# Kernel tuning notes

Hardware: AMD Instinct MI355X
Metric: run time of the kernel (lower is better)

The kernel has to match this reference:

```python
import jax, jax.numpy as jnp
import numpy as np

ALPHA = 0.5
BETA = 0.25
D_AGG = 0.5          # delta_aggregation
D_DIS = 3.0          # delta_discrimination
OHEM_RATIO = 3.0
MAX_INST = 8         # max instance label (labels in 1..MAX_INST, 0 = background)
SMOOTH = 1e-3


def _aggr_discr(text, kernel, embed):
    # text, kernel: [HW] int32 instance labels; embed: [4, HW] float
    inst = jnp.arange(1, MAX_INST + 1)                              # [I]
    kmask = (kernel[None, :] == inst[:, None]).astype(embed.dtype)  # [I, HW]
    tmask = (text[None, :] == inst[:, None]).astype(embed.dtype)   # [I, HW]
    kcnt = kmask.sum(1)                                             # [I]
    tcnt = tmask.sum(1)
    valid = ((kcnt > 0) & (tcnt > 0)).astype(embed.dtype)           # [I]
    # per-instance kernel-mean embedding (segment mean)
    avgs = (kmask @ embed.T) / jnp.maximum(kcnt, 1.0)[:, None]      # [I, 4]
    # aggregation: per-pixel distance to the mean of its text instance
    avgs_full = jnp.concatenate([jnp.zeros((1, 4), embed.dtype), avgs], 0)  # row 0 = bg
    pix_avg = avgs_full[text]                                       # [HW, 4]
    sq = jnp.sum((embed.T - pix_avg) ** 2, axis=1)
    dist = jnp.sqrt(sq + 1e-12) - D_AGG
    lg = jnp.log1p(jnp.maximum(dist, 0.0) ** 2)                     # [HW]
    aggr_i = (tmask @ lg) / jnp.maximum(tcnt, 1.0)                  # [I]
    n = valid.sum()
    loss_aggr = jnp.where(n > 0, (aggr_i * valid).sum() / jnp.maximum(n, 1.0), 0.0)
    # discrimination: pairwise hinge between valid kernel means
    pairv = jnp.triu(valid[:, None] * valid[None, :], k=1)          # [I, I]
    sq_ij = jnp.sum((avgs[:, None, :] - avgs[None, :, :]) ** 2, axis=-1)
    d_ij = jnp.sqrt(jnp.where(pairv > 0, sq_ij, 1.0))               # safe sqrt
    L = jnp.log1p(jnp.maximum(D_DIS - d_ij, 0.0) ** 2)
    denom = n * (n - 1)
    loss_discr = jnp.where(n > 1, (L * pairv).sum() / jnp.maximum(denom, 1.0), 0.0)
    return loss_aggr, loss_discr


def _ohem(score, gt_text, gt_mask):
    # score, gt_text, gt_mask: [HW] float
    pos = gt_text > 0.5
    maskpos = gt_mask > 0.5
    pos_num = (pos & maskpos).sum()
    neg = ~pos
    neg_num = jnp.minimum((pos_num * OHEM_RATIO).astype(jnp.int32), neg.sum())
    neg_sc = jnp.where(neg, score, -jnp.inf)
    srt = -jnp.sort(-neg_sc)                                        # descending
    thr = srt[jnp.clip(neg_num - 1, 0, score.shape[0] - 1)]
    samp = ((score >= thr) | pos) & maskpos
    fallback = (pos_num == 0) | (neg_num == 0)
    return jnp.where(fallback, maskpos, samp).astype(score.dtype)


def _dice(pred_logits, target, mask):
    # all [N, HW]
    p = jax.nn.sigmoid(pred_logits) * mask
    t = (target > 0.5).astype(p.dtype) * mask
    a = jnp.sum(p * t, 1) + SMOOTH
    b = jnp.sum(p * p, 1) + SMOOTH
    c = jnp.sum(t * t, 1) + SMOOTH
    return 1.0 - 2.0 * a / (b + c)


def reference(preds, gt_texts, gt_kernels, gt_mask):
    N, C, H, W = preds.shape
    HW = H * W
    pred_text = preds[:, 0].reshape(N, HW)
    pred_kernel = preds[:, 1].reshape(N, HW)
    embed = preds[:, 2:].reshape(N, 4, HW)
    t = gt_texts.reshape(N, HW)
    k = gt_kernels.reshape(N, HW)
    m = gt_mask.reshape(N, HW).astype(preds.dtype)
    tf = t.astype(preds.dtype)
    kf = k.astype(preds.dtype)
    loss_aggr, loss_discr = jax.vmap(_aggr_discr)(t, k, embed)
    samp = jax.vmap(_ohem)(jax.lax.stop_gradient(pred_text), tf, m)
    loss_text = _dice(pred_text, tf, samp)
    samp_k = (tf > 0.5).astype(preds.dtype) * m
    loss_kernel = _dice(pred_kernel, kf, samp_k)
    # reduction='mean' then coefs [1, alpha, beta, beta]
    return jnp.stack([
        loss_text.mean(),
        ALPHA * loss_kernel.mean(),
        BETA * loss_aggr.mean(),
        BETA * loss_discr.mean(),
    ])


def setup_inputs() -> dict:
    key = jax.random.key(0)
    k1, k2, k3, k4 = jax.random.split(key, 4)
    N, H, W = 16, 512, 512
    preds = jax.random.normal(k1, (N, 6, H, W), dtype=jnp.float32)
    gt_texts = jax.random.randint(k2, (N, H, W), 0, 9, dtype=jnp.int32)
    gt_kernels = jax.random.randint(k3, (N, H, W), 0, 9, dtype=jnp.int32)
    gt_mask = jax.random.randint(k4, (N, H, W), 0, 2, dtype=jnp.int32)
    return {"preds": preds, "gt_texts": gt_texts, "gt_kernels": gt_kernels, "gt_mask": gt_mask}
```

## Files before the change

### kernel.cpp

```cpp
#include <hip/hip_runtime.h>
#include <math.h>

#define HW (512 * 512)
#define NB 16
#define NTHR 256
#define GXS 64
#define CH 4
#define NSEG 256
#define SEGSZ 1024
#define REP 16

#define OFF_ACC    0
#define ACC_STRIDE (NB * 52)
#define OFF_PACC   (OFF_ACC + REP * ACC_STRIDE)
#define PACC_STRIDE (NB * 4)
#define OFF_HISTFB (OFF_PACC + REP * PACC_STRIDE)
#define OFF_NEGMX  (OFF_HISTFB + 4 * 16 * 256)
#define ZERO_WORDS (OFF_NEGMX + NB * REP)
#define OFF_TBL    ZERO_WORDS
#define OFF_THR    (OFF_TBL + 16 * 45)
#define OFF_FB     (OFF_THR + 16)
#define OFF_NVAL   (OFF_FB + 16)
#define OFF_DISCR  (OFF_NVAL + 16)
#define OFF_PREFIX (OFF_DISCR + 16)
#define OFF_KKC    (OFF_PREFIX + 16)
#define OFF_NEGC   (OFF_KKC + 16)
#define OFF_CNTS   (OFF_NEGC + 16)
#define OFF_KEYS   (OFF_CNTS + NB * NSEG)
#define WS_FULL_BYTES ((size_t)(OFF_KEYS + NB * HW) * 4)


__device__ __forceinline__ unsigned fmap(float f) {
    unsigned u = __float_as_uint(f);
    return (u & 0x80000000u) ? ~u : (u | 0x80000000u);
}
__device__ __forceinline__ float funmap(unsigned u) {
    return (u & 0x80000000u) ? __uint_as_float(u & 0x7FFFFFFFu)
                             : __uint_as_float(~u);
}
__device__ __forceinline__ float wred(float x) {
#pragma unroll
    for (int o = 32; o; o >>= 1) x += __shfl_xor(x, o);
    return x;
}
__device__ __forceinline__ unsigned wredu(unsigned x) {
#pragma unroll
    for (int o = 32; o; o >>= 1) x += __shfl_xor(x, o);
    return x;
}
__device__ __forceinline__ unsigned wredumax(unsigned x) {
#pragma unroll
    for (int o = 32; o; o >>= 1) x = max(x, (unsigned)__shfl_xor((int)x, o));
    return x;
}

__global__ __launch_bounds__(NTHR, 2) void k_stats(const float* __restrict__ preds,
                        const int* __restrict__ text,
                        const int* __restrict__ kern,
                        const int* __restrict__ mask,
                        unsigned* __restrict__ wsu, int do_compact) {
    float* wsf = (float*)wsu;
    const int b = blockIdx.y;
    const int tid = threadIdx.x;
    const int lane = tid & 63;
    const unsigned long long lmask = (1ull << lane) - 1ull;
    __shared__ float sacc[52];
    if (tid < 52) sacc[tid] = 0.f;
    __syncthreads();

    const int* tb = text + b * HW;
    const int* kb = kern + b * HW;
    const int* mb = mask + b * HW;
    const float* p0 = preds + (size_t)(b * 6 + 0) * HW;
    const float* p1 = preds + (size_t)(b * 6 + 1) * HW;
    const float* e0 = preds + (size_t)(b * 6 + 2) * HW;
    const float* e1 = e0 + HW;
    const float* e2 = e0 + 2 * HW;
    const float* e3 = e0 + 3 * HW;

    const int seg = blockIdx.x * 4 + (tid >> 6);
    unsigned* keys = wsu + OFF_KEYS + (size_t)b * HW + (size_t)seg * SEGSZ;
    unsigned segoff = 0;
    unsigned mkAll = 0u;

    float ks[32];
#pragma unroll
    for (int i = 0; i < 32; i++) ks[i] = 0.f;
    float r_ak = 0.f, r_bk = 0.f, r_ck = 0.f;
    unsigned kcW[8] = {0, 0, 0, 0, 0, 0, 0, 0};
    unsigned tcW[8] = {0, 0, 0, 0, 0, 0, 0, 0};
    unsigned posW = 0;

#pragma unroll 1
    for (int c = 0; c < CH; c++) {
        const int base = blockIdx.x * (NTHR * 4 * CH) + c * (NTHR * 4) + tid * 4;
        const int4 t4 = *(const int4*)(tb + base);
        const int4 k4 = *(const int4*)(kb + base);
        const int4 m4 = *(const int4*)(mb + base);
        const float4 s4 = *(const float4*)(p0 + base);
        const float4 q4 = *(const float4*)(p1 + base);
        const float4 a4 = *(const float4*)(e0 + base);
        const float4 b4 = *(const float4*)(e1 + base);
        const float4 c4 = *(const float4*)(e2 + base);
        const float4 d4 = *(const float4*)(e3 + base);

#define PIX(T, K, M, Q, A, B, C, D) do {                                     \
        bool pos_ = (T) > 0, mp_ = (M) > 0;                                  \
        float sm_ = (pos_ && mp_) ? 1.f : 0.f;                               \
        float sg_ = 1.f / (1.f + expf(-(Q)));                                \
        float ik_ = ((K) > 0) ? 1.f : 0.f;                                   \
        r_ak += sm_ * sg_ * ik_;                                             \
        r_bk += sm_ * sg_ * sg_;                                             \
        r_ck += sm_ * ik_;                                                   \
        posW += (unsigned)__popcll(__ballot(pos_ && mp_));                   \
        _Pragma("unroll")                                                    \
        for (int i_ = 0; i_ < 8; i_++) {                                     \
            bool hit_ = ((K) == i_ + 1);                                     \
            kcW[i_] += (unsigned)__popcll(__ballot(hit_));                   \
            tcW[i_] += (unsigned)__popcll(__ballot((T) == i_ + 1));          \
            float h_ = hit_ ? 1.f : 0.f;                                     \
            ks[i_ * 4 + 0] += h_ * (A);                                      \
            ks[i_ * 4 + 1] += h_ * (B);                                      \
            ks[i_ * 4 + 2] += h_ * (C);                                      \
            ks[i_ * 4 + 3] += h_ * (D);                                      \
        }                                                                    \
    } while (0)

        PIX(t4.x, k4.x, m4.x, q4.x, a4.x, b4.x, c4.x, d4.x);
        PIX(t4.y, k4.y, m4.y, q4.y, a4.y, b4.y, c4.y, d4.y);
        PIX(t4.z, k4.z, m4.z, q4.z, a4.z, b4.z, c4.z, d4.z);
        PIX(t4.w, k4.w, m4.w, q4.w, a4.w, b4.w, c4.w, d4.w);
#undef PIX

        const unsigned long long m0 = __ballot(t4.x == 0);
        const unsigned long long m1 = __ballot(t4.y == 0);
        const unsigned long long m2 = __ballot(t4.z == 0);
        const unsigned long long m3 = __ballot(t4.w == 0);
        const unsigned c0 = (unsigned)__popcll(m0), c1 = (unsigned)__popcll(m1);
        const unsigned c2 = (unsigned)__popcll(m2), c3 = (unsigned)__popcll(m3);
        if (do_compact) {
            if (t4.x == 0) keys[segoff + (unsigned)__popcll(m0 & lmask)] = fmap(s4.x);
            if (t4.y == 0) keys[segoff + c0 + (unsigned)__popcll(m1 & lmask)] = fmap(s4.y);
            if (t4.z == 0) keys[segoff + c0 + c1 + (unsigned)__popcll(m2 & lmask)] = fmap(s4.z);
            if (t4.w == 0) keys[segoff + c0 + c1 + c2 + (unsigned)__popcll(m3 & lmask)] = fmap(s4.w);
        }
        segoff += c0 + c1 + c2 + c3;
        unsigned mk = 0u;
        if (t4.x == 0) mk = max(mk, ~fmap(s4.x));
        if (t4.y == 0) mk = max(mk, ~fmap(s4.y));
        if (t4.z == 0) mk = max(mk, ~fmap(s4.z));
        if (t4.w == 0) mk = max(mk, ~fmap(s4.w));
        mkAll = max(mkAll, mk);
    }

    if (lane == 0) wsu[OFF_CNTS + b * NSEG + seg] = segoff;
    mkAll = wredumax(mkAll);
    if (lane == 0 && mkAll)
        atomicMax(&wsu[OFF_NEGMX + b * REP + (blockIdx.x & (REP - 1))], mkAll);

#pragma unroll
    for (int i = 0; i < 32; i++) {
        float v = wred(ks[i]);
        if (lane == 0) atomicAdd(&sacc[16 + i], v);
    }
    {
        float v = wred(r_ak); if (lane == 0) atomicAdd(&sacc[49], v);
        v = wred(r_bk); if (lane == 0) atomicAdd(&sacc[50], v);
        v = wred(r_ck); if (lane == 0) atomicAdd(&sacc[51], v);
    }
    if (lane == 0) {
#pragma unroll
        for (int i = 0; i < 8; i++) {
            atomicAdd(&sacc[i], (float)kcW[i]);
            atomicAdd(&sacc[8 + i], (float)tcW[i]);
        }
        atomicAdd(&sacc[48], (float)posW);
    }
    __syncthreads();
    if (tid < 52) {
        const int rep = blockIdx.x & (REP - 1);
        atomicAdd(&wsf[OFF_ACC + rep * ACC_STRIDE + b * 52 + tid], sacc[tid]);
    }
}

__global__ void k_sel(unsigned* __restrict__ wsu, int do_select) {
    float* wsf = (float*)wsu;
    const int b = blockIdx.x;
    const int tid = threadIdx.x;
    const int lane = tid & 63;
    __shared__ float s_acc[52];
    __shared__ float s_avg[8][4];
    __shared__ int s_valid[8];
    __shared__ unsigned s_hist[256];
    __shared__ unsigned s_negtot;
    __shared__ unsigned s_kk, s_prefix;

    if (tid < 52) {
        float v = 0.f;
#pragma unroll
        for (int r = 0; r < REP; r++) v += wsf[OFF_ACC + r * ACC_STRIDE + b * 52 + tid];
        s_acc[tid] = v;
    }
    if (tid == 0) s_negtot = 0u;
    __syncthreads();

    const unsigned myc = wsu[OFF_CNTS + b * NSEG + tid];
    {
        unsigned cw = wredu(myc);
        if (lane == 0) atomicAdd(&s_negtot, cw);
    }
    if (tid < 8) {
        float kcf = s_acc[tid];
        float tcf = s_acc[8 + tid];
        int valid = (kcf > 0.f && tcf > 0.f) ? 1 : 0;
        float inv = 1.f / fmaxf(kcf, 1.f);
        float w = valid ? 1.f / fmaxf(tcf, 1.f) : 0.f;
#pragma unroll
        for (int c = 0; c < 4; c++) {
            float a = s_acc[16 + tid * 4 + c] * inv;
            s_avg[tid][c] = a;
            wsf[OFF_TBL + b * 45 + (tid + 1) * 5 + c] = a;
        }
        s_valid[tid] = valid;
        wsf[OFF_TBL + b * 45 + (tid + 1) * 5 + 4] = w;
    }
    if (tid >= 8 && tid < 13) wsf[OFF_TBL + b * 45 + (tid - 8)] = 0.f;
    __syncthreads();
    if (tid == 0) {
        int nval = 0;
        for (int i = 0; i < 8; i++) nval += s_valid[i];
        float L = 0.f;
        for (int i = 0; i < 8; i++)
            for (int j = i + 1; j < 8; j++)
                if (s_valid[i] && s_valid[j]) {
                    float sq = 0.f;
                    for (int c = 0; c < 4; c++) {
                        float d = s_avg[i][c] - s_avg[j][c];
                        sq += d * d;
                    }
                    float h = fmaxf(3.0f - sqrtf(sq), 0.f);
                    L += log1pf(h * h);
                }
        wsf[OFF_DISCR + b] = (nval > 1) ? L / fmaxf((float)(nval * (nval - 1)), 1.f) : 0.f;
        wsu[OFF_NVAL + b] = (unsigned)nval;
        unsigned pos = (unsigned)s_acc[48];
        unsigned neg = s_negtot;
        wsu[OFF_NEGC + b] = neg;
        unsigned nn = min(pos * 3u, neg);
        int fb = (pos == 0u || nn == 0u) ? 1 : 0;
        wsu[OFF_FB + b] = (unsigned)fb;
        wsu[OFF_KKC + b] = fb ? 0u : nn;
        wsu[OFF_PREFIX + b] = 0u;
        wsf[OFF_THR + b] = 0.f;
        unsigned kk = fb ? 0u : nn;
        if (!fb && nn == neg) {
            unsigned mx = 0u;
#pragma unroll
            for (int r = 0; r < REP; r++) mx = max(mx, wsu[OFF_NEGMX + b * REP + r]);
            wsf[OFF_THR + b] = funmap(~mx);
            kk = 0u;
        }
        s_kk = kk;
        s_prefix = 0u;
    }
    __syncthreads();
    if (!do_select) return;
    if (s_kk == 0u) return;
    const unsigned* keys = wsu + OFF_KEYS + (size_t)b * HW + (size_t)tid * SEGSZ;
    unsigned prefix = 0u;
    for (int pass = 0; pass < 4; pass++) {
        const int shift = 24 - 8 * pass;
        const unsigned fmask = (pass == 0) ? 0u : (0xFFFFFFFFu << (shift + 8));
        s_hist[tid] = 0u;
        __syncthreads();
        for (unsigned i = 0; i < myc; i++) {
            unsigned key = keys[i];
            if ((key & fmask) == prefix) atomicAdd(&s_hist[(key >> shift) & 255u], 1u);
        }
        __syncthreads();
        if (tid == 0) {
            unsigned k2 = s_kk;
            for (int bin = 255; bin >= 0; --bin) {
                unsigned c = s_hist[bin];
                if (k2 <= c) { s_prefix = prefix | (((unsigned)bin) << shift); s_kk = k2; break; }
                k2 -= c;
            }
        }
        __syncthreads();
        prefix = s_prefix;
    }
    if (tid == 0) wsf[OFF_THR + b] = funmap(prefix);
}

__global__ void k_hist(const float* __restrict__ preds, const int* __restrict__ text,
                       unsigned* __restrict__ wsu, int pass) {
    const int b = blockIdx.y;
    const int tid = threadIdx.x;
    __shared__ unsigned h[256];
    h[tid] = 0u;
    __syncthreads();
    const unsigned prefix = wsu[OFF_PREFIX + b];
    const int shift = 24 - 8 * pass;
    const unsigned fmask = (pass == 0) ? 0u : (0xFFFFFFFFu << (shift + 8));
    const int* tb = text + b * HW;
    const float* pt = preds + (size_t)(b * 6) * HW;
    for (int p = blockIdx.x * NTHR + tid; p < HW; p += gridDim.x * NTHR) {
        if (tb[p] == 0) {
            unsigned key = fmap(pt[p]);
            if ((key & fmask) == prefix) atomicAdd(&h[(key >> shift) & 255u], 1u);
        }
    }
    __syncthreads();
    if (h[tid]) atomicAdd(&wsu[OFF_HISTFB + pass * 4096 + b * 256 + tid], h[tid]);
}
__global__ void k_select(unsigned* __restrict__ wsu, int pass) {
    int b = threadIdx.x;
    if (b >= NB) return;
    float* wsf = (float*)wsu;
    unsigned k = wsu[OFF_KKC + b];
    unsigned prefix = wsu[OFF_PREFIX + b];
    const int shift = 24 - 8 * pass;
    const unsigned* h = &wsu[OFF_HISTFB + pass * 4096 + b * 256];
    if (k > 0) {
        for (int bin = 255; bin >= 0; --bin) {
            unsigned c = h[bin];
            if (k <= c) { prefix |= ((unsigned)bin) << shift; break; }
            k -= c;
        }
        wsu[OFF_KKC + b] = k;
        wsu[OFF_PREFIX + b] = prefix;
    }
    if (pass == 3) wsf[OFF_THR + b] = funmap(prefix);
}

__global__ __launch_bounds__(NTHR, 2) void k_pix(const float* __restrict__ preds,
                      const int* __restrict__ text,
                      const int* __restrict__ mask,
                      unsigned* __restrict__ wsu) {
    float* wsf = (float*)wsu;
    const int b = blockIdx.y;
    const int tid = threadIdx.x;
    const int lane = tid & 63;
    __shared__ float stbl[45];
    __shared__ float sred[4];
    __shared__ float sthr;
    __shared__ unsigned sfb;
    if (tid < 45) stbl[tid] = wsf[OFF_TBL + b * 45 + tid];
    if (tid < 4) sred[tid] = 0.f;
    if (tid == 0) { sthr = wsf[OFF_THR + b]; sfb = wsu[OFF_FB + b]; }
    __syncthreads();
    const float thr = sthr;
    const bool fb = sfb != 0u;
    float r_at = 0.f, r_bt = 0.f, r_ct = 0.f, r_ag = 0.f;
    const int* tb = text + b * HW;
    const int* mb = mask + b * HW;
    const float* p0 = preds + (size_t)(b * 6) * HW;
    const float* e0 = preds + (size_t)(b * 6 + 2) * HW;
    const float* e1 = e0 + HW;
    const float* e2 = e0 + 2 * HW;
    const float* e3 = e0 + 3 * HW;

#pragma unroll 1
    for (int c = 0; c < CH; c++) {
        const int base = blockIdx.x * (NTHR * 4 * CH) + c * (NTHR * 4) + tid * 4;
        const int4 t4 = *(const int4*)(tb + base);
        const int4 m4 = *(const int4*)(mb + base);
        const float4 s4 = *(const float4*)(p0 + base);
        const float4 a4 = *(const float4*)(e0 + base);
        const float4 b4 = *(const float4*)(e1 + base);
        const float4 c4 = *(const float4*)(e2 + base);
        const float4 d4 = *(const float4*)(e3 + base);

#define PPIX(T, M, S, A, B, C, D) do {                                       \
        bool pos_ = (T) > 0;                                                 \
        bool samp_ = fb ? ((M) > 0) : ((((S) >= thr) || pos_) && ((M) > 0)); \
        float sg_ = 1.f / (1.f + expf(-(S)));                                \
        float smf_ = samp_ ? 1.f : 0.f;                                      \
        float it_ = pos_ ? 1.f : 0.f;                                        \
        r_at += smf_ * sg_ * it_;                                            \
        r_bt += smf_ * sg_ * sg_;                                            \
        r_ct += smf_ * it_;                                                  \
        int t5_ = min((T), 8) * 5;                                           \
        float d0_ = (A) - stbl[t5_ + 0];                                     \
        float d1_ = (B) - stbl[t5_ + 1];                                     \
        float d2_ = (C) - stbl[t5_ + 2];                                     \
        float d3_ = (D) - stbl[t5_ + 3];                                     \
        float w_ = stbl[t5_ + 4];                                            \
        float sq_ = d0_ * d0_ + d1_ * d1_ + d2_ * d2_ + d3_ * d3_;           \
        float dist_ = sqrtf(sq_ + 1e-12f) - 0.5f;                            \
        float hp_ = fmaxf(dist_, 0.f);                                       \
        r_ag += w_ * log1pf(hp_ * hp_);                                      \
    } while (0)

        PPIX(t4.x, m4.x, s4.x, a4.x, b4.x, c4.x, d4.x);
        PPIX(t4.y, m4.y, s4.y, a4.y, b4.y, c4.y, d4.y);
        PPIX(t4.z, m4.z, s4.z, a4.z, b4.z, c4.z, d4.z);
        PPIX(t4.w, m4.w, s4.w, a4.w, b4.w, c4.w, d4.w);
#undef PPIX
    }

    {
        float v = wred(r_at); if (lane == 0) atomicAdd(&sred[0], v);
        v = wred(r_bt); if (lane == 0) atomicAdd(&sred[1], v);
        v = wred(r_ct); if (lane == 0) atomicAdd(&sred[2], v);
        v = wred(r_ag); if (lane == 0) atomicAdd(&sred[3], v);
    }
    __syncthreads();
    if (tid < 4) {
        const int rep = blockIdx.x & (REP - 1);
        atomicAdd(&wsf[OFF_PACC + rep * PACC_STRIDE + b * 4 + tid], sred[tid]);
    }
}

__global__ void k_final(unsigned* __restrict__ wsu, float* __restrict__ out) {
    float* wsf = (float*)wsu;
    __shared__ float lt[NB], lk[NB], la[NB], ld[NB];
    int b = threadIdx.x;
    if (b < NB) {
        const float S = 1e-3f;
        float ak = 0.f, bk = 0.f, ck = 0.f, at = 0.f, bt = 0.f, ct = 0.f, ag = 0.f;
#pragma unroll
        for (int r = 0; r < REP; r++) {
            ak += wsf[OFF_ACC + r * ACC_STRIDE + b * 52 + 49];
            bk += wsf[OFF_ACC + r * ACC_STRIDE + b * 52 + 50];
            ck += wsf[OFF_ACC + r * ACC_STRIDE + b * 52 + 51];
            at += wsf[OFF_PACC + r * PACC_STRIDE + b * 4 + 0];
            bt += wsf[OFF_PACC + r * PACC_STRIDE + b * 4 + 1];
            ct += wsf[OFF_PACC + r * PACC_STRIDE + b * 4 + 2];
            ag += wsf[OFF_PACC + r * PACC_STRIDE + b * 4 + 3];
        }
        lt[b] = 1.f - 2.f * (at + S) / ((bt + S) + (ct + S));
        lk[b] = 1.f - 2.f * (ak + S) / ((bk + S) + (ck + S));
        int nval = (int)wsu[OFF_NVAL + b];
        la[b] = (nval > 0) ? ag / fmaxf((float)nval, 1.f) : 0.f;
        ld[b] = wsf[OFF_DISCR + b];
    }
    __syncthreads();
    if (b == 0) {
        float st = 0, sk = 0, sa = 0, sd = 0;
        for (int i = 0; i < NB; i++) { st += lt[i]; sk += lk[i]; sa += la[i]; sd += ld[i]; }
        out[0] = st / NB;
        out[1] = 0.5f * sk / NB;
        out[2] = 0.25f * sa / NB;
        out[3] = 0.25f * sd / NB;
    }
}

extern "C" void kernel_launch(void* const* d_in, const int* in_sizes, int n_in,
                              void* d_out, int out_size, void* d_ws, size_t ws_size,
                              hipStream_t stream) {
    const float* preds = (const float*)d_in[0];
    const int* text = (const int*)d_in[1];
    const int* kern = (const int*)d_in[2];
    const int* mask = (const int*)d_in[3];
    unsigned* wsu = (unsigned*)d_ws;
    float* out = (float*)d_out;

    const int do_compact = (ws_size >= WS_FULL_BYTES) ? 1 : 0;

    hipMemsetAsync(d_ws, 0, (size_t)ZERO_WORDS * 4, stream);

    dim3 grid(GXS, NB);
    k_stats<<<grid, NTHR, 0, stream>>>(preds, text, kern, mask, wsu, do_compact);
    k_sel<<<NB, NTHR, 0, stream>>>(wsu, do_compact);
    if (!do_compact) {
        dim3 hgrid(128, NB);
        for (int pass = 0; pass < 4; pass++) {
            k_hist<<<hgrid, NTHR, 0, stream>>>(preds, text, wsu, pass);
            k_select<<<1, 64, 0, stream>>>(wsu, pass);
        }
    }
    k_pix<<<grid, NTHR, 0, stream>>>(preds, text, mask, wsu);
    k_final<<<1, 64, 0, stream>>>(wsu, out);
}
```

Before: 244.7 us.

## Fold selection and final reduction into last-block epilogues, drop key compaction

The separate selection kernel and final kernel are merged into the stats and pixel kernels. A per-batch ticket counter lets the last finishing block of k_stats compute means, the discrimination loss and the OHEM threshold, and a global ticket lets the last k_pix block produce the output. The compacted negative-key buffer and the multi-launch histogram fallback are removed. Per-block partials are now written to private slots, and the negative count is carried through the accumulator. The cost is that the rare exact top-k path now scans the full image in a single block per batch.

```diff
diff --git a/kernel.cpp b/kernel.cpp
--- a/kernel.cpp
+++ b/kernel.cpp
@@ -6,28 +6,22 @@
 #define NTHR 256
 #define GXS 64
 #define CH 4
-#define NSEG 256
-#define SEGSZ 1024
-#define REP 16
+#define PREP 4
+#define ACCW 56
 
 #define OFF_ACC    0
-#define ACC_STRIDE (NB * 52)
-#define OFF_PACC   (OFF_ACC + REP * ACC_STRIDE)
-#define PACC_STRIDE (NB * 4)
-#define OFF_HISTFB (OFF_PACC + REP * PACC_STRIDE)
-#define OFF_NEGMX  (OFF_HISTFB + 4 * 16 * 256)
-#define ZERO_WORDS (OFF_NEGMX + NB * REP)
-#define OFF_TBL    ZERO_WORDS
-#define OFF_THR    (OFF_TBL + 16 * 45)
-#define OFF_FB     (OFF_THR + 16)
-#define OFF_NVAL   (OFF_FB + 16)
-#define OFF_DISCR  (OFF_NVAL + 16)
-#define OFF_PREFIX (OFF_DISCR + 16)
-#define OFF_KKC    (OFF_PREFIX + 16)
-#define OFF_NEGC   (OFF_KKC + 16)
-#define OFF_CNTS   (OFF_NEGC + 16)
-#define OFF_KEYS   (OFF_CNTS + NB * NSEG)
-#define WS_FULL_BYTES ((size_t)(OFF_KEYS + NB * HW) * 4)
+#define OFF_NEGMX  (OFF_ACC + NB * GXS * ACCW)
+#define OFF_PACC   (OFF_NEGMX + NB)
+#define OFF_TICKS  (OFF_PACC + PREP * NB * 4)
+#define OFF_TICK2  (OFF_TICKS + NB)
+#define ZERO_OFF   OFF_NEGMX
+#define ZERO_WORDS (NB + PREP * NB * 4 + NB + 1)
+#define OFF_KDICE  (OFF_TICK2 + 1)
+#define OFF_TBL    (OFF_KDICE + NB * 3)
+#define OFF_THR    (OFF_TBL + NB * 45)
+#define OFF_FB     (OFF_THR + NB)
+#define OFF_NVAL   (OFF_FB + NB)
+#define OFF_DISCR  (OFF_NVAL + NB)
 
 
 __device__ __forceinline__ unsigned fmap(float f) {
@@ -43,29 +37,34 @@
     for (int o = 32; o; o >>= 1) x += __shfl_xor(x, o);
     return x;
 }
-__device__ __forceinline__ unsigned wredu(unsigned x) {
-#pragma unroll
-    for (int o = 32; o; o >>= 1) x += __shfl_xor(x, o);
-    return x;
-}
 __device__ __forceinline__ unsigned wredumax(unsigned x) {
 #pragma unroll
     for (int o = 32; o; o >>= 1) x = max(x, (unsigned)__shfl_xor((int)x, o));
     return x;
+}
+__device__ __forceinline__ float agent_loadf(const float* p) {
+    return __hip_atomic_load(p, __ATOMIC_RELAXED, __HIP_MEMORY_SCOPE_AGENT);
 }
 
 __global__ __launch_bounds__(NTHR, 2) void k_stats(const float* __restrict__ preds,
                         const int* __restrict__ text,
                         const int* __restrict__ kern,
                         const int* __restrict__ mask,
-                        unsigned* __restrict__ wsu, int do_compact) {
+                        unsigned* __restrict__ wsu) {
     float* wsf = (float*)wsu;
     const int b = blockIdx.y;
     const int tid = threadIdx.x;
     const int lane = tid & 63;
-    const unsigned long long lmask = (1ull << lane) - 1ull;
-    __shared__ float sacc[52];
-    if (tid < 52) sacc[tid] = 0.f;
+    __shared__ float sacc[53];
+    __shared__ unsigned smx;
+    __shared__ unsigned s_last;
+    __shared__ float s_sum[53];
+    __shared__ float s_avg[8][4];
+    __shared__ int s_valid[8];
+    __shared__ unsigned s_hist[256];
+    __shared__ unsigned s_kk, s_prefix;
+    if (tid < 53) sacc[tid] = 0.f;
+    if (tid == 0) smx = 0u;
     __syncthreads();
 
     const int* tb = text + b * HW;
@@ -78,9 +77,7 @@
     const float* e2 = e0 + 2 * HW;
     const float* e3 = e0 + 3 * HW;
 
-    const int seg = blockIdx.x * 4 + (tid >> 6);
-    unsigned* keys = wsu + OFF_KEYS + (size_t)b * HW + (size_t)seg * SEGSZ;
-    unsigned segoff = 0;
+    unsigned negc = 0u;
     unsigned mkAll = 0u;
 
     float ks[32];
@@ -132,19 +129,10 @@
         PIX(t4.w, k4.w, m4.w, q4.w, a4.w, b4.w, c4.w, d4.w);
 #undef PIX
 
-        const unsigned long long m0 = __ballot(t4.x == 0);
-        const unsigned long long m1 = __ballot(t4.y == 0);
-        const unsigned long long m2 = __ballot(t4.z == 0);
-        const unsigned long long m3 = __ballot(t4.w == 0);
-        const unsigned c0 = (unsigned)__popcll(m0), c1 = (unsigned)__popcll(m1);
-        const unsigned c2 = (unsigned)__popcll(m2), c3 = (unsigned)__popcll(m3);
-        if (do_compact) {
-            if (t4.x == 0) keys[segoff + (unsigned)__popcll(m0 & lmask)] = fmap(s4.x);
-            if (t4.y == 0) keys[segoff + c0 + (unsigned)__popcll(m1 & lmask)] = fmap(s4.y);
-            if (t4.z == 0) keys[segoff + c0 + c1 + (unsigned)__popcll(m2 & lmask)] = fmap(s4.z);
-            if (t4.w == 0) keys[segoff + c0 + c1 + c2 + (unsigned)__popcll(m3 & lmask)] = fmap(s4.w);
-        }
-        segoff += c0 + c1 + c2 + c3;
+        negc += (unsigned)__popcll(__ballot(t4.x == 0));
+        negc += (unsigned)__popcll(__ballot(t4.y == 0));
+        negc += (unsigned)__popcll(__ballot(t4.z == 0));
+        negc += (unsigned)__popcll(__ballot(t4.w == 0));
         unsigned mk = 0u;
         if (t4.x == 0) mk = max(mk, ~fmap(s4.x));
         if (t4.y == 0) mk = max(mk, ~fmap(s4.y));
@@ -153,10 +141,8 @@
         mkAll = max(mkAll, mk);
     }
 
-    if (lane == 0) wsu[OFF_CNTS + b * NSEG + seg] = segoff;
     mkAll = wredumax(mkAll);
-    if (lane == 0 && mkAll)
-        atomicMax(&wsu[OFF_NEGMX + b * REP + (blockIdx.x & (REP - 1))], mkAll);
+    if (lane == 0) atomicMax(&smx, mkAll);
 
 #pragma unroll
     for (int i = 0; i < 32; i++) {
@@ -175,49 +161,39 @@
             atomicAdd(&sacc[8 + i], (float)tcW[i]);
         }
         atomicAdd(&sacc[48], (float)posW);
-    }
-    __syncthreads();
-    if (tid < 52) {
-        const int rep = blockIdx.x & (REP - 1);
-        atomicAdd(&wsf[OFF_ACC + rep * ACC_STRIDE + b * 52 + tid], sacc[tid]);
-    }
-}
-
-__global__ void k_sel(unsigned* __restrict__ wsu, int do_select) {
-    float* wsf = (float*)wsu;
-    const int b = blockIdx.x;
-    const int tid = threadIdx.x;
-    const int lane = tid & 63;
-    __shared__ float s_acc[52];
-    __shared__ float s_avg[8][4];
-    __shared__ int s_valid[8];
-    __shared__ unsigned s_hist[256];
-    __shared__ unsigned s_negtot;
-    __shared__ unsigned s_kk, s_prefix;
-
-    if (tid < 52) {
+        atomicAdd(&sacc[52], (float)negc);
+    }
+    __syncthreads();
+    if (tid < 53)
+        wsf[OFF_ACC + (b * GXS + blockIdx.x) * ACCW + tid] = sacc[tid];
+    if (tid == 0 && smx) atomicMax(&wsu[OFF_NEGMX + b], smx);
+    __threadfence();
+    __syncthreads();
+    if (tid == 0) {
+        unsigned t = atomicAdd(&wsu[OFF_TICKS + b], 1u);
+        s_last = (t == (unsigned)(GXS - 1)) ? 1u : 0u;
+    }
+    __syncthreads();
+    if (!s_last) return;
+
+    __threadfence();
+    if (tid < 53) {
         float v = 0.f;
-#pragma unroll
-        for (int r = 0; r < REP; r++) v += wsf[OFF_ACC + r * ACC_STRIDE + b * 52 + tid];
-        s_acc[tid] = v;
-    }
-    if (tid == 0) s_negtot = 0u;
-    __syncthreads();
-
-    const unsigned myc = wsu[OFF_CNTS + b * NSEG + tid];
-    {
-        unsigned cw = wredu(myc);
-        if (lane == 0) atomicAdd(&s_negtot, cw);
-    }
+        const float* p = wsf + OFF_ACC + (size_t)b * GXS * ACCW + tid;
+#pragma unroll 8
+        for (int r = 0; r < GXS; r++) v += agent_loadf(p + r * ACCW);
+        s_sum[tid] = v;
+    }
+    __syncthreads();
     if (tid < 8) {
-        float kcf = s_acc[tid];
-        float tcf = s_acc[8 + tid];
+        float kcf = s_sum[tid];
+        float tcf = s_sum[8 + tid];
         int valid = (kcf > 0.f && tcf > 0.f) ? 1 : 0;
         float inv = 1.f / fmaxf(kcf, 1.f);
         float w = valid ? 1.f / fmaxf(tcf, 1.f) : 0.f;
 #pragma unroll
         for (int c = 0; c < 4; c++) {
-            float a = s_acc[16 + tid * 4 + c] * inv;
+            float a = s_sum[16 + tid * 4 + c] * inv;
             s_avg[tid][c] = a;
             wsf[OFF_TBL + b * 45 + (tid + 1) * 5 + c] = a;
         }
@@ -225,6 +201,9 @@
         wsf[OFF_TBL + b * 45 + (tid + 1) * 5 + 4] = w;
     }
     if (tid >= 8 && tid < 13) wsf[OFF_TBL + b * 45 + (tid - 8)] = 0.f;
+    if (tid >= 16 && tid < 19) wsf[OFF_KDICE + b * 3 + (tid - 16)] = s_sum[49 + (tid - 16)];
+    if (tid < PREP * 4)
+        wsf[OFF_PACC + ((tid >> 2) * NB + b) * 4 + (tid & 3)] = 0.f;
     __syncthreads();
     if (tid == 0) {
         int nval = 0;
@@ -243,39 +222,35 @@
                 }
         wsf[OFF_DISCR + b] = (nval > 1) ? L / fmaxf((float)(nval * (nval - 1)), 1.f) : 0.f;
         wsu[OFF_NVAL + b] = (unsigned)nval;
-        unsigned pos = (unsigned)s_acc[48];
-        unsigned neg = s_negtot;
-        wsu[OFF_NEGC + b] = neg;
+        unsigned pos = (unsigned)s_sum[48];
+        unsigned neg = (unsigned)s_sum[52];
         unsigned nn = min(pos * 3u, neg);
         int fb = (pos == 0u || nn == 0u) ? 1 : 0;
         wsu[OFF_FB + b] = (unsigned)fb;
-        wsu[OFF_KKC + b] = fb ? 0u : nn;
-        wsu[OFF_PREFIX + b] = 0u;
         wsf[OFF_THR + b] = 0.f;
         unsigned kk = fb ? 0u : nn;
         if (!fb && nn == neg) {
-            unsigned mx = 0u;
-#pragma unroll
-            for (int r = 0; r < REP; r++) mx = max(mx, wsu[OFF_NEGMX + b * REP + r]);
-            wsf[OFF_THR + b] = funmap(~mx);
+            unsigned nm = (unsigned)__hip_atomic_load(&wsu[OFF_NEGMX + b],
+                              __ATOMIC_RELAXED, __HIP_MEMORY_SCOPE_AGENT);
+            wsf[OFF_THR + b] = funmap(~nm);
             kk = 0u;
         }
         s_kk = kk;
         s_prefix = 0u;
     }
     __syncthreads();
-    if (!do_select) return;
     if (s_kk == 0u) return;
-    const unsigned* keys = wsu + OFF_KEYS + (size_t)b * HW + (size_t)tid * SEGSZ;
     unsigned prefix = 0u;
     for (int pass = 0; pass < 4; pass++) {
         const int shift = 24 - 8 * pass;
         const unsigned fmask = (pass == 0) ? 0u : (0xFFFFFFFFu << (shift + 8));
         s_hist[tid] = 0u;
         __syncthreads();
-        for (unsigned i = 0; i < myc; i++) {
-            unsigned key = keys[i];
-            if ((key & fmask) == prefix) atomicAdd(&s_hist[(key >> shift) & 255u], 1u);
+        for (int p = tid; p < HW; p += NTHR) {
+            if (tb[p] == 0) {
+                unsigned key = fmap(p0[p]);
+                if ((key & fmask) == prefix) atomicAdd(&s_hist[(key >> shift) & 255u], 1u);
+            }
         }
         __syncthreads();
         if (tid == 0) {
@@ -292,51 +267,11 @@
     if (tid == 0) wsf[OFF_THR + b] = funmap(prefix);
 }
 
-__global__ void k_hist(const float* __restrict__ preds, const int* __restrict__ text,
-                       unsigned* __restrict__ wsu, int pass) {
-    const int b = blockIdx.y;
-    const int tid = threadIdx.x;
-    __shared__ unsigned h[256];
-    h[tid] = 0u;
-    __syncthreads();
-    const unsigned prefix = wsu[OFF_PREFIX + b];
-    const int shift = 24 - 8 * pass;
-    const unsigned fmask = (pass == 0) ? 0u : (0xFFFFFFFFu << (shift + 8));
-    const int* tb = text + b * HW;
-    const float* pt = preds + (size_t)(b * 6) * HW;
-    for (int p = blockIdx.x * NTHR + tid; p < HW; p += gridDim.x * NTHR) {
-        if (tb[p] == 0) {
-            unsigned key = fmap(pt[p]);
-            if ((key & fmask) == prefix) atomicAdd(&h[(key >> shift) & 255u], 1u);
-        }
-    }
-    __syncthreads();
-    if (h[tid]) atomicAdd(&wsu[OFF_HISTFB + pass * 4096 + b * 256 + tid], h[tid]);
-}
-__global__ void k_select(unsigned* __restrict__ wsu, int pass) {
-    int b = threadIdx.x;
-    if (b >= NB) return;
-    float* wsf = (float*)wsu;
-    unsigned k = wsu[OFF_KKC + b];
-    unsigned prefix = wsu[OFF_PREFIX + b];
-    const int shift = 24 - 8 * pass;
-    const unsigned* h = &wsu[OFF_HISTFB + pass * 4096 + b * 256];
-    if (k > 0) {
-        for (int bin = 255; bin >= 0; --bin) {
-            unsigned c = h[bin];
-            if (k <= c) { prefix |= ((unsigned)bin) << shift; break; }
-            k -= c;
-        }
-        wsu[OFF_KKC + b] = k;
-        wsu[OFF_PREFIX + b] = prefix;
-    }
-    if (pass == 3) wsf[OFF_THR + b] = funmap(prefix);
-}
-
 __global__ __launch_bounds__(NTHR, 2) void k_pix(const float* __restrict__ preds,
                       const int* __restrict__ text,
                       const int* __restrict__ mask,
-                      unsigned* __restrict__ wsu) {
+                      unsigned* __restrict__ wsu,
+                      float* __restrict__ out) {
     float* wsf = (float*)wsu;
     const int b = blockIdx.y;
     const int tid = threadIdx.x;
@@ -345,6 +280,9 @@
     __shared__ float sred[4];
     __shared__ float sthr;
     __shared__ unsigned sfb;
+    __shared__ unsigned s_last;
+    __shared__ float sfin[64];
+    __shared__ float lt[NB], lk[NB], la[NB], ld[NB];
     if (tid < 45) stbl[tid] = wsf[OFF_TBL + b * 45 + tid];
     if (tid < 4) sred[tid] = 0.f;
     if (tid == 0) { sthr = wsf[OFF_THR + b]; sfb = wsu[OFF_FB + b]; }
@@ -407,36 +345,40 @@
     }
     __syncthreads();
     if (tid < 4) {
-        const int rep = blockIdx.x & (REP - 1);
-        atomicAdd(&wsf[OFF_PACC + rep * PACC_STRIDE + b * 4 + tid], sred[tid]);
-    }
-}
-
-__global__ void k_final(unsigned* __restrict__ wsu, float* __restrict__ out) {
-    float* wsf = (float*)wsu;
-    __shared__ float lt[NB], lk[NB], la[NB], ld[NB];
-    int b = threadIdx.x;
-    if (b < NB) {
+        const int rep = blockIdx.x & (PREP - 1);
+        atomicAdd(&wsf[OFF_PACC + (rep * NB + b) * 4 + tid], sred[tid]);
+    }
+    __threadfence();
+    if (tid == 0) {
+        unsigned t = atomicAdd(&wsu[OFF_TICK2], 1u);
+        s_last = (t == (unsigned)(GXS * NB - 1)) ? 1u : 0u;
+    }
+    __syncthreads();
+    if (!s_last) return;
+    if (tid < 64) {
+        const int bb = tid >> 2, v = tid & 3;
+        float s = 0.f;
+#pragma unroll
+        for (int r = 0; r < PREP; r++)
+            s += atomicAdd(&wsf[OFF_PACC + (r * NB + bb) * 4 + v], 0.f);
+        sfin[tid] = s;
+    }
+    __syncthreads();
+    if (tid < NB) {
         const float S = 1e-3f;
-        float ak = 0.f, bk = 0.f, ck = 0.f, at = 0.f, bt = 0.f, ct = 0.f, ag = 0.f;
-#pragma unroll
-        for (int r = 0; r < REP; r++) {
-            ak += wsf[OFF_ACC + r * ACC_STRIDE + b * 52 + 49];
-            bk += wsf[OFF_ACC + r * ACC_STRIDE + b * 52 + 50];
-            ck += wsf[OFF_ACC + r * ACC_STRIDE + b * 52 + 51];
-            at += wsf[OFF_PACC + r * PACC_STRIDE + b * 4 + 0];
-            bt += wsf[OFF_PACC + r * PACC_STRIDE + b * 4 + 1];
-            ct += wsf[OFF_PACC + r * PACC_STRIDE + b * 4 + 2];
-            ag += wsf[OFF_PACC + r * PACC_STRIDE + b * 4 + 3];
-        }
-        lt[b] = 1.f - 2.f * (at + S) / ((bt + S) + (ct + S));
-        lk[b] = 1.f - 2.f * (ak + S) / ((bk + S) + (ck + S));
-        int nval = (int)wsu[OFF_NVAL + b];
-        la[b] = (nval > 0) ? ag / fmaxf((float)nval, 1.f) : 0.f;
-        ld[b] = wsf[OFF_DISCR + b];
-    }
-    __syncthreads();
-    if (b == 0) {
+        float at = sfin[tid * 4 + 0], bt = sfin[tid * 4 + 1];
+        float ct = sfin[tid * 4 + 2], ag = sfin[tid * 4 + 3];
+        float ak = wsf[OFF_KDICE + tid * 3 + 0];
+        float bk = wsf[OFF_KDICE + tid * 3 + 1];
+        float ck = wsf[OFF_KDICE + tid * 3 + 2];
+        lt[tid] = 1.f - 2.f * (at + S) / ((bt + S) + (ct + S));
+        lk[tid] = 1.f - 2.f * (ak + S) / ((bk + S) + (ck + S));
+        int nval = (int)wsu[OFF_NVAL + tid];
+        la[tid] = (nval > 0) ? ag / fmaxf((float)nval, 1.f) : 0.f;
+        ld[tid] = wsf[OFF_DISCR + tid];
+    }
+    __syncthreads();
+    if (tid == 0) {
         float st = 0, sk = 0, sa = 0, sd = 0;
         for (int i = 0; i < NB; i++) { st += lt[i]; sk += lk[i]; sa += la[i]; sd += ld[i]; }
         out[0] = st / NB;
@@ -456,20 +398,10 @@
     unsigned* wsu = (unsigned*)d_ws;
     float* out = (float*)d_out;
 
-    const int do_compact = (ws_size >= WS_FULL_BYTES) ? 1 : 0;
-
-    hipMemsetAsync(d_ws, 0, (size_t)ZERO_WORDS * 4, stream);
+    (void)hipMemsetAsync((char*)d_ws + (size_t)ZERO_OFF * 4, 0,
+                         (size_t)ZERO_WORDS * 4, stream);
 
     dim3 grid(GXS, NB);
-    k_stats<<<grid, NTHR, 0, stream>>>(preds, text, kern, mask, wsu, do_compact);
-    k_sel<<<NB, NTHR, 0, stream>>>(wsu, do_compact);
-    if (!do_compact) {
-        dim3 hgrid(128, NB);
-        for (int pass = 0; pass < 4; pass++) {
-            k_hist<<<hgrid, NTHR, 0, stream>>>(preds, text, wsu, pass);
-            k_select<<<1, 64, 0, stream>>>(wsu, pass);
-        }
-    }
-    k_pix<<<grid, NTHR, 0, stream>>>(preds, text, mask, wsu);
-    k_final<<<1, 64, 0, stream>>>(wsu, out);
-}
+    k_stats<<<grid, NTHR, 0, stream>>>(preds, text, kern, mask, wsu);
+    k_pix<<<grid, NTHR, 0, stream>>>(preds, text, mask, wsu, out);
+}
```

Result: slower. 422.4 us (+72.6%).
